# Performance work log

Measured on AMD Instinct MI355X. Metric: run time of the kernel, lower is better.

## Reference

```python
import jax, jax.numpy as jnp
import numpy as np

N_NODES = 100000
N_EDGES = 600000
D_FEAT = 128
HID = 128


def setup_inputs() -> dict:
    key = jax.random.key(0)
    ks = jax.random.split(key, 8)
    zi = jax.random.normal(ks[0], (N_NODES, D_FEAT), dtype=jnp.float32)
    zj = jax.random.normal(ks[1], (N_NODES, D_FEAT), dtype=jnp.float32)
    src = jax.random.randint(ks[2], (N_EDGES,), 0, N_NODES, dtype=jnp.int64 if jax.config.jax_enable_x64 else jnp.int32)
    dst = jax.random.randint(ks[3], (N_EDGES,), 0, N_NODES, dtype=jnp.int64 if jax.config.jax_enable_x64 else jnp.int32)
    W1 = jax.random.normal(ks[4], (2 * D_FEAT, HID), dtype=jnp.float32) * (1.0 / np.sqrt(2 * D_FEAT))
    b1 = jnp.zeros((HID,), dtype=jnp.float32)
    W3 = jax.random.normal(ks[5], (HID, 1), dtype=jnp.float32) * (1.0 / np.sqrt(HID))
    b3 = jnp.zeros((1,), dtype=jnp.float32)
    return {"zi": zi, "zj": zj, "src": src, "dst": dst,
            "W1": W1, "b1": b1, "W3": W3, "b3": b3}


def reference(zi, zj, src, dst, W1, b1, W3, b3):
    # Irregular gather: per-edge src/dst node features, then concat -> [E, 2*d]
    hi = zi[src]              # [E, d]
    hj = zj[dst]              # [E, d]
    raw = jnp.concatenate([hi, hj], axis=1)  # [E, 2d]
    # LR_Classification with n_layers=2: only linear_1 and linear_3 run
    # (the linear_2 loop executes n_layers-2 = 0 times); dropout is identity (eval).
    hid = jax.nn.relu(raw @ W1 + b1)          # [E, HID]
    logit = hid @ W3 + b3                     # [E, 1]
    return jax.nn.sigmoid(logit)
```

## Files before the change

### kernel.cpp

```cpp
#include <hip/hip_runtime.h>
#include <hip/hip_bf16.h>

typedef __attribute__((ext_vector_type(8))) short short8;
typedef __attribute__((ext_vector_type(4))) float f32x4;
typedef __attribute__((ext_vector_type(4))) unsigned int u32x4;
typedef __attribute__((ext_vector_type(2))) unsigned int u32x2;

#define DFEAT 128
#define LDW 136

__device__ __forceinline__ unsigned short f2bf(float f) {
    unsigned int u = __float_as_uint(f);
    u += 0x7FFFu + ((u >> 16) & 1u);
    return (unsigned short)(u >> 16);
}
__device__ __forceinline__ unsigned int cvt2(float lo, float hi) {
    unsigned int r;
    asm("v_cvt_pk_bf16_f32 %0, %1, %2" : "=v"(r) : "v"(lo), "v"(hi));
    return r;
}
__device__ __forceinline__ float bf2f(unsigned int bits) {
    return __uint_as_float(bits << 16);
}

__device__ __forceinline__ void pf_issue(f32x4 (&pf)[8], const float* zr) {
    asm volatile("global_load_dwordx4 %0, %1, off"            : "=&v"(pf[0]) : "v"(zr) : "memory");
    asm volatile("global_load_dwordx4 %0, %1, off offset:16"  : "=&v"(pf[1]) : "v"(zr) : "memory");
    asm volatile("global_load_dwordx4 %0, %1, off offset:128" : "=&v"(pf[2]) : "v"(zr) : "memory");
    asm volatile("global_load_dwordx4 %0, %1, off offset:144" : "=&v"(pf[3]) : "v"(zr) : "memory");
    asm volatile("global_load_dwordx4 %0, %1, off offset:256" : "=&v"(pf[4]) : "v"(zr) : "memory");
    asm volatile("global_load_dwordx4 %0, %1, off offset:272" : "=&v"(pf[5]) : "v"(zr) : "memory");
    asm volatile("global_load_dwordx4 %0, %1, off offset:384" : "=&v"(pf[6]) : "v"(zr) : "memory");
    asm volatile("global_load_dwordx4 %0, %1, off offset:400" : "=&v"(pf[7]) : "v"(zr) : "memory");
}

__global__ __launch_bounds__(256) void node_gemm(
    const float* __restrict__ zi, const float* __restrict__ zj,
    const float* __restrict__ W1, const float* __restrict__ b1,
    unsigned short* __restrict__ Aout, unsigned short* __restrict__ Bout,
    int nN)
{
    __shared__ unsigned short Wt[128][LDW];
    __shared__ float bias_lds[128];
    const int table = blockIdx.y;
    const float* __restrict__ z = table ? zj : zi;
    unsigned short* __restrict__ outp = table ? Bout : Aout;

    for (int idx = threadIdx.x; idx < 128 * 128; idx += 256) {
        int c = idx & 127, k = idx >> 7;
        Wt[c][k] = f2bf(W1[(size_t)(table * 128 + k) * DFEAT + c]);
    }
    if (threadIdx.x < 128) bias_lds[threadIdx.x] = table ? 0.f : b1[threadIdx.x];
    __syncthreads();

    const int lane = threadIdx.x & 63;
    const int l15  = lane & 15;
    const int kg   = lane >> 4;
    const int wv = blockIdx.x * 4 + (threadIdx.x >> 6);
    const int nw = gridDim.x * 4;
    const int nStrips = (nN + 15) >> 4;

    f32x4 pf[8];
    int s = wv;
    if (s < nStrips) {
        int row = s * 16 + l15;
        pf_issue(pf, z + (size_t)(row < nN ? row : nN - 1) * DFEAT + kg * 8);
    }
    asm volatile("s_waitcnt vmcnt(0)" ::: "memory");
    __builtin_amdgcn_sched_barrier(0);

    while (s < nStrips) {
        short8 bf[4];
#pragma unroll
        for (int kk = 0; kk < 4; ++kk) {
            union { unsigned int u[4]; short8 s8; } cv;
            cv.u[0] = cvt2(pf[2 * kk][0], pf[2 * kk][1]);
            cv.u[1] = cvt2(pf[2 * kk][2], pf[2 * kk][3]);
            cv.u[2] = cvt2(pf[2 * kk + 1][0], pf[2 * kk + 1][1]);
            cv.u[3] = cvt2(pf[2 * kk + 1][2], pf[2 * kk + 1][3]);
            bf[kk] = cv.s8;
        }
        __builtin_amdgcn_sched_barrier(0);

        int sp = s + nw;
        if (sp < nStrips) {
            int row = sp * 16 + l15;
            pf_issue(pf, z + (size_t)(row < nN ? row : nN - 1) * DFEAT + kg * 8);
        }
        __builtin_amdgcn_sched_barrier(0);

        int row = s * 16 + l15;
        unsigned short* op = outp + (size_t)row * DFEAT + kg * 4;
#pragma unroll
        for (int h = 0; h < 2; ++h) {
            f32x4 acc[4];
#pragma unroll
            for (int ci = 0; ci < 4; ++ci)
                acc[ci] = *(const f32x4*)&bias_lds[(h * 4 + ci) * 16 + kg * 4];
#pragma unroll
            for (int kk = 0; kk < 4; ++kk) {
#pragma unroll
                for (int ci = 0; ci < 4; ++ci) {
                    short8 a = *(const short8*)&Wt[(h * 4 + ci) * 16 + l15][kk * 32 + kg * 8];
                    acc[ci] = __builtin_amdgcn_mfma_f32_16x16x32_bf16(a, bf[kk], acc[ci], 0, 0, 0);
                }
            }
            if (row < nN) {
#pragma unroll
                for (int ci = 0; ci < 4; ++ci) {
                    u32x2 v;
                    v[0] = cvt2(acc[ci][0], acc[ci][1]);
                    v[1] = cvt2(acc[ci][2], acc[ci][3]);
                    *(u32x2*)(op + (h * 4 + ci) * 16) = v;
                }
            }
        }
        s = sp;
        asm volatile("s_waitcnt vmcnt(8)" ::: "memory");
        __builtin_amdgcn_sched_barrier(0);
    }
}

__global__ __launch_bounds__(256) void edge_kernel(
    const unsigned short* __restrict__ A, const unsigned short* __restrict__ B,
    const int* __restrict__ src, const int* __restrict__ dst,
    const float* __restrict__ W3, const float* __restrict__ b3,
    float* __restrict__ out, int nE)
{
    const int lane = threadIdx.x & 63;
    const int sub  = lane & 15;
    const int grp  = lane >> 4;

    float w3v[8];
#pragma unroll
    for (int j = 0; j < 8; ++j) w3v[j] = W3[sub * 8 + j];
    const float bb = b3[0];

    int wv = blockIdx.x * 4 + (threadIdx.x >> 6);
    int nw = gridDim.x * 4;

    for (int base = wv * 8; base < nE; base += nw * 8) {
        int e0 = base + grp;
        int e1 = base + 4 + grp;
        bool v0 = e0 < nE, v1 = e1 < nE;
        int s0 = v0 ? src[e0] : 0, d0 = v0 ? dst[e0] : 0;
        int s1 = v1 ? src[e1] : 0, d1 = v1 ? dst[e1] : 0;

        const u32x4* pa0 = (const u32x4*)(A + (size_t)s0 * DFEAT + sub * 8);
        const u32x4* pb0 = (const u32x4*)(B + (size_t)d0 * DFEAT + sub * 8);
        const u32x4* pa1 = (const u32x4*)(A + (size_t)s1 * DFEAT + sub * 8);
        const u32x4* pb1 = (const u32x4*)(B + (size_t)d1 * DFEAT + sub * 8);
        u32x4 av0 = *pa0, bv0 = *pb0;
        u32x4 av1 = *pa1, bv1 = *pb1;

        float p0 = 0.f, p1 = 0.f;
#pragma unroll
        for (int w = 0; w < 4; ++w) {
            float x0 = fmaxf(bf2f(av0[w] & 0xFFFFu) + bf2f(bv0[w] & 0xFFFFu), 0.f);
            float x1 = fmaxf(bf2f(av0[w] >> 16)     + bf2f(bv0[w] >> 16),     0.f);
            p0 = fmaf(x0, w3v[w * 2], p0);
            p0 = fmaf(x1, w3v[w * 2 + 1], p0);
            float y0 = fmaxf(bf2f(av1[w] & 0xFFFFu) + bf2f(bv1[w] & 0xFFFFu), 0.f);
            float y1 = fmaxf(bf2f(av1[w] >> 16)     + bf2f(bv1[w] >> 16),     0.f);
            p1 = fmaf(y0, w3v[w * 2], p1);
            p1 = fmaf(y1, w3v[w * 2 + 1], p1);
        }
#pragma unroll
        for (int off = 8; off > 0; off >>= 1) {
            p0 += __shfl_xor(p0, off, 64);
            p1 += __shfl_xor(p1, off, 64);
        }
        if (sub == 0) {
            if (v0) out[e0] = 1.f / (1.f + __expf(-(p0 + bb)));
            if (v1) out[e1] = 1.f / (1.f + __expf(-(p1 + bb)));
        }
    }
}

__global__ __launch_bounds__(256) void fallback_kernel(
    const float* __restrict__ zi, const float* __restrict__ zj,
    const int* __restrict__ src, const int* __restrict__ dst,
    const float* __restrict__ W1, const float* __restrict__ b1,
    const float* __restrict__ W3, const float* __restrict__ b3,
    float* __restrict__ out, int nE)
{
    int e = blockIdx.x * blockDim.x + threadIdx.x;
    if (e >= nE) return;
    const float* a = zi + (size_t)src[e] * DFEAT;
    const float* b = zj + (size_t)dst[e] * DFEAT;
    float logit = b3[0];
    for (int h = 0; h < 128; ++h) {
        float acc = b1[h];
        for (int k = 0; k < 128; ++k) acc = fmaf(a[k], W1[(size_t)k * 128 + h], acc);
        for (int k = 0; k < 128; ++k) acc = fmaf(b[k], W1[(size_t)(128 + k) * 128 + h], acc);
        if (acc > 0.f) logit = fmaf(acc, W3[h], logit);
    }
    out[e] = 1.f / (1.f + __expf(-logit));
}

extern "C" void kernel_launch(void* const* d_in, const int* in_sizes, int n_in,
                              void* d_out, int out_size, void* d_ws, size_t ws_size,
                              hipStream_t stream) {
    const float* zi = (const float*)d_in[0];
    const float* zj = (const float*)d_in[1];
    const int*  src = (const int*)d_in[2];
    const int*  dst = (const int*)d_in[3];
    const float* W1 = (const float*)d_in[4];
    const float* b1 = (const float*)d_in[5];
    const float* W3 = (const float*)d_in[6];
    const float* b3 = (const float*)d_in[7];
    float* out = (float*)d_out;

    int nN = in_sizes[0] / DFEAT;
    int nE = in_sizes[2];
    size_t abytes = (size_t)nN * DFEAT * sizeof(unsigned short);

    if (ws_size >= 2 * abytes) {
        unsigned short* A = (unsigned short*)d_ws;
        unsigned short* B = A + (size_t)nN * DFEAT;
        dim3 g1(256, 2, 1);
        node_gemm<<<g1, 256, 0, stream>>>(zi, zj, W1, b1, A, B, nN);
        edge_kernel<<<2048, 256, 0, stream>>>(A, B, src, dst, W3, b3, out, nE);
    } else {
        fallback_kernel<<<(nE + 255) / 256, 256, 0, stream>>>(
            zi, zj, src, dst, W1, b1, W3, b3, out, nE);
    }
}
```

Before: 79.47 us.

## Double-buffer node feature prefetch in node_gemm and double its grid

```diff
diff --git a/kernel.cpp b/kernel.cpp
--- a/kernel.cpp
+++ b/kernel.cpp
@@ -59,17 +59,20 @@
     const int wv = blockIdx.x * 4 + (threadIdx.x >> 6);
     const int nw = gridDim.x * 4;
     const int nStrips = (nN + 15) >> 4;
-
-    f32x4 pf[8];
-    int s = wv;
-    if (s < nStrips) {
+    if (wv >= nStrips) return;
+
+    auto zaddr = [&](int s) {
         int row = s * 16 + l15;
-        pf_issue(pf, z + (size_t)(row < nN ? row : nN - 1) * DFEAT + kg * 8);
-    }
-    asm volatile("s_waitcnt vmcnt(0)" ::: "memory");
-    __builtin_amdgcn_sched_barrier(0);
-
-    while (s < nStrips) {
+        if (row >= nN) row = nN - 1;
+        return z + (size_t)row * DFEAT + kg * 8;
+    };
+
+    f32x4 pfA[8], pfB[8];
+    int sA = wv, sB = wv + nw;
+    pf_issue(pfA, zaddr(sA));
+    pf_issue(pfB, zaddr(sB));
+
+    auto process = [&](f32x4 (&pf)[8], int s, int spre) {
         short8 bf[4];
 #pragma unroll
         for (int kk = 0; kk < 4; ++kk) {
@@ -81,14 +84,8 @@
             bf[kk] = cv.s8;
         }
         __builtin_amdgcn_sched_barrier(0);
-
-        int sp = s + nw;
-        if (sp < nStrips) {
-            int row = sp * 16 + l15;
-            pf_issue(pf, z + (size_t)(row < nN ? row : nN - 1) * DFEAT + kg * 8);
-        }
-        __builtin_amdgcn_sched_barrier(0);
-
+        pf_issue(pf, zaddr(spre));
+        __builtin_amdgcn_sched_barrier(0);
         int row = s * 16 + l15;
         unsigned short* op = outp + (size_t)row * DFEAT + kg * 4;
 #pragma unroll
@@ -115,9 +112,25 @@
                 }
             }
         }
-        s = sp;
-        asm volatile("s_waitcnt vmcnt(8)" ::: "memory");
-        __builtin_amdgcn_sched_barrier(0);
+    };
+
+    asm volatile("s_waitcnt vmcnt(8)" ::: "memory");
+    __builtin_amdgcn_sched_barrier(0);
+    process(pfA, sA, sA + 2 * nw);
+    asm volatile("s_waitcnt vmcnt(16)" ::: "memory");
+    __builtin_amdgcn_sched_barrier(0);
+    process(pfB, sB, sB + 2 * nw);
+    sA += 2 * nw; sB += 2 * nw;
+
+    while (sA < nStrips) {
+        asm volatile("s_waitcnt vmcnt(24)" ::: "memory");
+        __builtin_amdgcn_sched_barrier(0);
+        process(pfA, sA, sA + 2 * nw);
+        sA += 2 * nw;
+        asm volatile("s_waitcnt vmcnt(24)" ::: "memory");
+        __builtin_amdgcn_sched_barrier(0);
+        process(pfB, sB, sB + 2 * nw);
+        sB += 2 * nw;
     }
 }
 
@@ -218,7 +231,7 @@
     if (ws_size >= 2 * abytes) {
         unsigned short* A = (unsigned short*)d_ws;
         unsigned short* B = A + (size_t)nN * DFEAT;
-        dim3 g1(256, 2, 1);
+        dim3 g1(512, 2, 1);
         node_gemm<<<g1, 256, 0, stream>>>(zi, zj, W1, b1, A, B, nN);
         edge_kernel<<<2048, 256, 0, stream>>>(A, B, src, dst, W3, b3, out, nE);
     } else {
```

Result: slower. 84.35 us (+6.1%).
